# Optimization experiments

Measured on AMD Instinct MI355X. Metric: run time of the kernel, lower is better.

## Reference

```python
import jax, jax.numpy as jnp
import numpy as np

TEMP = 20.0     # args.temp
ATT_WT = 0.3    # args.att_wt
EPS = 1e-12     # torch F.normalize eps

L, B, C, H, W = 3, 2, 2048, 60, 60   # 3 layer4 bottleneck maps
CH = 256                              # merged feature channels for f_q/f_s


def setup_inputs() -> dict:
    key = jax.random.key(0)
    k1, k2, k3, k4, k5 = jax.random.split(key, 5)
    return {
        "fq_feats": jax.random.normal(k1, (L, B, C, H, W), dtype=jnp.float32),
        "fs_feats": jax.random.normal(k2, (L, B, C, H, W), dtype=jnp.float32),
        "f_q": jax.random.normal(k3, (B, CH, H, W), dtype=jnp.float32),
        "f_s": jax.random.normal(k4, (B, CH, H, W), dtype=jnp.float32),
        "corr_weight": jax.random.normal(k5, (L,), dtype=jnp.float32),
    }


def _l2_normalize(x, axis):
    # torch F.normalize(dim=1): x / max(||x||, eps)
    n = jnp.sqrt(jnp.sum(x * x, axis=axis, keepdims=True))
    return x / jnp.maximum(n, EPS)


def reference(fq_feats, fs_feats, f_q, f_s, corr_weight):
    b, ch, h, w = f_q.shape
    hw = h * w
    # per-scale channel-wise L2 normalize (cosine correlation)
    fqn = _l2_normalize(fq_feats, axis=2)   # [L,B,C,H,W]
    fsn = _l2_normalize(fs_feats, axis=2)
    # get_corr: pairwise cosine similarity volume per scale -> [B, L, hw_q, hw_s]
    fq_flat = fqn.reshape(fqn.shape[0], b, fqn.shape[2], hw)  # [L,B,C,hw]
    fs_flat = fsn.reshape(fsn.shape[0], b, fsn.shape[2], hw)
    corr = jnp.einsum('lbcq,lbcs->blqs', fq_flat, fs_flat)    # [B,L,hw,hw]
    # MatchNet corr_forward: 1x1 conv reducing match_ch -> 1, softmax over
    # support positions (scaled by temp), attend into v = f_s
    red = jnp.einsum('l,blqs->bqs', corr_weight, corr)        # [B,hw,hw]
    attn = jax.nn.softmax(red * TEMP, axis=-1)                # over support hw
    v = f_s.reshape(b, ch, hw)                                # [B,ch,hw]
    att_fq = jnp.einsum('bqs,bcs->bcq', attn, v).reshape(b, ch, h, w)
    fq = (f_q + att_fq * ATT_WT) / (1.0 + ATT_WT)
    return fq, att_fq
```

## Files before the change

### kernel.cpp

```cpp
#include <hip/hip_runtime.h>
#include <hip/hip_bf16.h>
#include <stdint.h>

#define L3D 3
#define BD 2
#define CD 2048
#define HW 3600
#define CH 256
#define HWP 3712
#define KD 6144
#define SP 3712
#define LB6 6
#define NPLANE 12
#define NT 48

typedef __attribute__((ext_vector_type(8))) short short8;
typedef __attribute__((ext_vector_type(4))) float f32x4;
typedef __attribute__((ext_vector_type(4))) int i32x4;
typedef __attribute__((ext_vector_type(8))) int i32x8;

__device__ __forceinline__ short f2bf(float v) {
  uint32_t x = __float_as_uint(v);
  uint32_t r = (x + 0x7FFFu + ((x >> 16) & 1u)) >> 16;
  return (short)(r & 0xFFFFu);
}

__device__ __forceinline__ float bf2f(short s) {
  return __uint_as_float(((uint32_t)(uint16_t)s) << 16);
}

__device__ __forceinline__ void load_lds16(const void* g, void* l) {
  __builtin_amdgcn_global_load_lds(
      (const __attribute__((address_space(1))) void*)g,
      (__attribute__((address_space(3))) void*)l, 16, 0, 0);
}

__global__ __launch_bounds__(256) void fnt_k(const float* __restrict__ fq,
                                             const float* __restrict__ fs,
                                             const float* __restrict__ cw,
                                             uint8_t* __restrict__ An,
                                             uint8_t* __restrict__ Bn) {
  const int j = blockIdx.y;
  const int qt = blockIdx.x * 64;
  const bool isq = (j < LB6);
  const int lb = isq ? j : j - LB6;
  const int l = lb / BD, b = lb % BD;
  const float* x = (isq ? fq : fs) + (size_t)lb * CD * HW;
  uint8_t* dst = isq ? An : Bn;

  const int tid = threadIdx.x;
  const int tx = tid & 63, part = tid >> 6;
  const int q = qt + tx;

  float s0 = 0.f, s1 = 0.f, s2 = 0.f, s3 = 0.f;
  if (q < HW) {
    const float* p = x + (size_t)part * 512 * HW + q;
    for (int c = 0; c < 512; c += 4) {
      float v0 = p[(size_t)(c + 0) * HW];
      float v1 = p[(size_t)(c + 1) * HW];
      float v2 = p[(size_t)(c + 2) * HW];
      float v3 = p[(size_t)(c + 3) * HW];
      s0 += v0 * v0; s1 += v1 * v1; s2 += v2 * v2; s3 += v3 * v3;
    }
  }
  __shared__ float buf[256];
  __shared__ float ivs[64];
  buf[tid] = (s0 + s1) + (s2 + s3);
  __syncthreads();
  if (tid < 64) {
    float t = buf[tid] + buf[tid + 64] + buf[tid + 128] + buf[tid + 192];
    const float scale = isq ? (cw[l] * 32.0f) : 32.0f;
    ivs[tid] = (1.f / fmaxf(sqrtf(t), 1e-12f)) * scale;
  }

  __shared__ float tile[64][65];
  const int wx = tid & 7, wy = tid >> 3;
  for (int ct = 0; ct < 32; ct++) {
    const float* px = x + (size_t)ct * 64 * HW;
    __syncthreads();
#pragma unroll
    for (int r = 0; r < 16; r++) {
      int cl = r * 4 + part;
      tile[cl][tx] = (q < HW) ? px[(size_t)cl * HW + q] : 0.f;
    }
    __syncthreads();
#pragma unroll
    for (int it = 0; it < 2; it++) {
      int qrow = wy + it * 32;
      int qq = qt + qrow;
      if (qq < HW) {
        float iv = ivs[qrow];
        float v[8];
#pragma unroll
        for (int jj = 0; jj < 8; jj++) v[jj] = tile[wx * 8 + jj][qrow] * iv;
        int lo = 0, hi = 0;
        lo = __builtin_amdgcn_cvt_pk_fp8_f32(v[0], v[1], lo, false);
        lo = __builtin_amdgcn_cvt_pk_fp8_f32(v[2], v[3], lo, true);
        hi = __builtin_amdgcn_cvt_pk_fp8_f32(v[4], v[5], hi, false);
        hi = __builtin_amdgcn_cvt_pk_fp8_f32(v[6], v[7], hi, true);
        int2 pk = make_int2(lo, hi);
        *reinterpret_cast<int2*>(dst + ((size_t)b * HWP + qq) * KD +
                                 (size_t)l * CD + ct * 64 + wx * 8) = pk;
      }
    }
  }
}

__global__ __launch_bounds__(512, 2) void gemm_main(const uint8_t* __restrict__ A,
                                                    const uint8_t* __restrict__ B,
                                                    __hip_bfloat16* __restrict__ C) {
  const int bz = blockIdx.y;
  const int lin = blockIdx.x;
  const int m_t = lin / 15, n_t = lin % 15;
  const int m0 = m_t * 256, n0 = n_t * 256;
  const int tid = threadIdx.x;
  const int lane = tid & 63;
  const int wv = tid >> 6;

  __shared__ uint8_t lA[2][256 * 128];
  __shared__ uint8_t lB[2][256 * 128];

  const uint8_t* gA = A + (size_t)bz * HWP * KD;
  const uint8_t* gB = B + (size_t)bz * HWP * KD;

  const int r_loc = tid >> 3;
  const int slot = tid & 7;
  const int csw = (slot - r_loc) & 7;
  const int wavebase = (tid & ~63) * 16;

  const int wr = (wv >> 2) * 128;
  const int wc = (wv & 3) * 64;
  const int ml = lane & 15;
  const int kg = lane >> 4;

  f32x4 acc[8][4];
#pragma unroll
  for (int i = 0; i < 8; i++)
#pragma unroll
    for (int jj = 0; jj < 4; jj++) acc[i][jj] = (f32x4){0.f, 0.f, 0.f, 0.f};

  auto stage = [&](int t, int bufi) {
    const int k0 = t * 128;
#pragma unroll
    for (int i = 0; i < 4; i++) {
      load_lds16(gA + (size_t)(m0 + i * 64 + r_loc) * KD + k0 + csw * 16,
                 &lA[bufi][i * 8192 + wavebase]);
      load_lds16(gB + (size_t)(n0 + i * 64 + r_loc) * KD + k0 + csw * 16,
                 &lB[bufi][i * 8192 + wavebase]);
    }
  };

  auto rdfrag = [&](const uint8_t* base, int row) -> i32x8 {
    const uint8_t* rp = base + (row << 7);
    i32x4 lo = *reinterpret_cast<const i32x4*>(rp + (((kg * 2)     + row) & 7) * 16);
    i32x4 hi = *reinterpret_cast<const i32x4*>(rp + (((kg * 2 + 1) + row) & 7) * 16);
    return __builtin_shufflevector(lo, hi, 0, 1, 2, 3, 4, 5, 6, 7);
  };

  stage(0, 0);
  asm volatile("s_waitcnt vmcnt(0)" ::: "memory");
  __builtin_amdgcn_s_barrier();

  for (int t = 0; t < NT; t++) {
    const int cur = t & 1;
    const uint8_t* pA = lA[cur];
    const uint8_t* pB = lB[cur];
    const bool st = (t + 1 < NT);
    i32x8 af[4], bfr[4];

#pragma unroll
    for (int x = 0; x < 4; x++) af[x] = rdfrag(pA, wr + x * 16 + ml);
#pragma unroll
    for (int x = 0; x < 2; x++) bfr[x] = rdfrag(pB, wc + x * 16 + ml);
    if (st) stage(t + 1, cur ^ 1);
    __builtin_amdgcn_s_barrier();
    asm volatile("s_waitcnt lgkmcnt(0)");
    __builtin_amdgcn_s_setprio(1);
#pragma unroll
    for (int mt = 0; mt < 4; mt++)
#pragma unroll
      for (int nt = 0; nt < 2; nt++)
        acc[mt][nt] = __builtin_amdgcn_mfma_scale_f32_16x16x128_f8f6f4(
            af[mt], bfr[nt], acc[mt][nt], 0, 0, 0, 0x7F7F7F7F, 0, 0x7F7F7F7F);
    __builtin_amdgcn_s_setprio(0);
    __builtin_amdgcn_s_barrier();

#pragma unroll
    for (int x = 2; x < 4; x++) bfr[x] = rdfrag(pB, wc + x * 16 + ml);
    __builtin_amdgcn_s_barrier();
    asm volatile("s_waitcnt lgkmcnt(0)");
    __builtin_amdgcn_s_setprio(1);
#pragma unroll
    for (int mt = 0; mt < 4; mt++)
#pragma unroll
      for (int nt = 2; nt < 4; nt++)
        acc[mt][nt] = __builtin_amdgcn_mfma_scale_f32_16x16x128_f8f6f4(
            af[mt], bfr[nt], acc[mt][nt], 0, 0, 0, 0x7F7F7F7F, 0, 0x7F7F7F7F);
    __builtin_amdgcn_s_setprio(0);
    __builtin_amdgcn_s_barrier();

#pragma unroll
    for (int x = 0; x < 4; x++) af[x] = rdfrag(pA, wr + 64 + x * 16 + ml);
    __builtin_amdgcn_s_barrier();
    asm volatile("s_waitcnt lgkmcnt(0)");
    __builtin_amdgcn_s_setprio(1);
#pragma unroll
    for (int mt = 0; mt < 4; mt++)
#pragma unroll
      for (int nt = 2; nt < 4; nt++)
        acc[4 + mt][nt] = __builtin_amdgcn_mfma_scale_f32_16x16x128_f8f6f4(
            af[mt], bfr[nt], acc[4 + mt][nt], 0, 0, 0, 0x7F7F7F7F, 0, 0x7F7F7F7F);
    __builtin_amdgcn_s_setprio(0);
    __builtin_amdgcn_s_barrier();

    __builtin_amdgcn_s_barrier();
    __builtin_amdgcn_s_setprio(1);
#pragma unroll
    for (int mt = 0; mt < 4; mt++)
#pragma unroll
      for (int nt = 0; nt < 2; nt++)
        acc[4 + mt][nt] = __builtin_amdgcn_mfma_scale_f32_16x16x128_f8f6f4(
            af[mt], bfr[nt], acc[4 + mt][nt], 0, 0, 0, 0x7F7F7F7F, 0, 0x7F7F7F7F);
    __builtin_amdgcn_s_setprio(0);
    if (st) asm volatile("s_waitcnt vmcnt(0)" ::: "memory");
    __builtin_amdgcn_s_barrier();
  }

  __hip_bfloat16* oc = C + (size_t)bz * HWP * SP;
  const int rq = (lane >> 4) * 4;
  const int cl = lane & 15;
#pragma unroll
  for (int mt = 0; mt < 8; mt++) {
    const int rb = m0 + wr + mt * 16 + rq;
#pragma unroll
    for (int nt = 0; nt < 4; nt++) {
      const int col = n0 + wc + nt * 16 + cl;
      if (col < SP) {
        f32x4 v = acc[mt][nt];
#pragma unroll
        for (int r = 0; r < 4; r++) {
          const int rr = rb + r;
          if (rr < HW) *reinterpret_cast<short*>(&oc[(size_t)rr * SP + col]) = f2bf(v[r]);
        }
      }
    }
  }
}

__global__ __launch_bounds__(256) void softmax_k(const __hip_bfloat16* __restrict__ red,
                                                 __hip_bfloat16* __restrict__ attn) {
  const int q = blockIdx.x;
  const int b = blockIdx.y;
  const __hip_bfloat16* row = red + ((size_t)b * HWP + q) * SP;
  __hip_bfloat16* orow = attn + ((size_t)b * HWP + q) * SP;
  const int tid = threadIdx.x;
  const int lane = tid & 63, wv = tid >> 6;
  const float SM = 20.0f / 1024.0f;

  float v0[8], v1[8];
  const int c1 = 256 + tid;
  const bool has1 = (c1 < 450);

  float mx = -3.4e38f;
  {
    short8 pk = *reinterpret_cast<const short8*>(&row[(size_t)tid * 8]);
#pragma unroll
    for (int j = 0; j < 8; j++) { v0[j] = bf2f(pk[j]); mx = fmaxf(mx, v0[j]); }
  }
  if (has1) {
    short8 pk = *reinterpret_cast<const short8*>(&row[(size_t)c1 * 8]);
#pragma unroll
    for (int j = 0; j < 8; j++) { v1[j] = bf2f(pk[j]); mx = fmaxf(mx, v1[j]); }
  }
  for (int off = 32; off > 0; off >>= 1) mx = fmaxf(mx, __shfl_down(mx, off, 64));
  __shared__ float sm[4];
  if (lane == 0) sm[wv] = mx;
  __syncthreads();
  mx = fmaxf(fmaxf(sm[0], sm[1]), fmaxf(sm[2], sm[3]));

  float sum = 0.f;
#pragma unroll
  for (int j = 0; j < 8; j++) { float e = __expf((v0[j] - mx) * SM); v0[j] = e; sum += e; }
  if (has1) {
#pragma unroll
    for (int j = 0; j < 8; j++) { float e = __expf((v1[j] - mx) * SM); v1[j] = e; sum += e; }
  }
  for (int off = 32; off > 0; off >>= 1) sum += __shfl_down(sum, off, 64);
  __syncthreads();
  if (lane == 0) sm[wv] = sum;
  __syncthreads();
  const float inv = 1.f / (sm[0] + sm[1] + sm[2] + sm[3]);

  {
    short8 o;
#pragma unroll
    for (int j = 0; j < 8; j++) o[j] = f2bf(v0[j] * inv);
    *reinterpret_cast<short8*>(&orow[(size_t)tid * 8]) = o;
  }
  if (has1) {
    short8 o;
#pragma unroll
    for (int j = 0; j < 8; j++) o[j] = f2bf(v1[j] * inv);
    *reinterpret_cast<short8*>(&orow[(size_t)c1 * 8]) = o;
  } else if (c1 < 464) {
    short8 z = {0, 0, 0, 0, 0, 0, 0, 0};
    *reinterpret_cast<short8*>(&orow[(size_t)c1 * 8]) = z;
  }
}

__global__ __launch_bounds__(256) void castv_k(const float* __restrict__ fs,
                                               __hip_bfloat16* __restrict__ vb) {
  const int idx = blockIdx.x * 256 + threadIdx.x;
  if (idx >= BD * CH * SP) return;
  const int s = idx % SP;
  const int bc = idx / SP;
  float v = (s < HW) ? fs[(size_t)bc * HW + s] : 0.f;
  *reinterpret_cast<short*>(&vb[idx]) = f2bf(v);
}

__global__ __launch_bounds__(256, 2) void pv_gemm(const __hip_bfloat16* __restrict__ A,
                                                  const __hip_bfloat16* __restrict__ B,
                                                  const float* __restrict__ fqin,
                                                  float* __restrict__ out) {
  const int bz = blockIdx.z;
  const int m0 = blockIdx.y * 128;
  const int n0 = blockIdx.x * 64;
  const int tid = threadIdx.x;
  const int lane = tid & 63;
  const int wv = tid >> 6;

  __shared__ __hip_bfloat16 lA[128 * 32];
  __shared__ __hip_bfloat16 lB[64 * 32];

  const __hip_bfloat16* gA = A + (size_t)bz * CH * SP;
  const __hip_bfloat16* gB = B + (size_t)bz * HWP * SP;

  const int r0 = tid >> 2;
  const int kc = (tid & 3) * 8;
  const int wb = (tid & ~63) * 8;

  const int wr = (wv >> 1) * 64;
  const int wc = (wv & 1) * 32;
  const int ml = lane & 15;
  const int kq = (lane >> 4) * 8;

  f32x4 acc[4][2];
#pragma unroll
  for (int i = 0; i < 4; i++)
#pragma unroll
    for (int jj = 0; jj < 2; jj++) acc[i][jj] = (f32x4){0.f, 0.f, 0.f, 0.f};

  for (int k0 = 0; k0 < SP; k0 += 32) {
    const __hip_bfloat16* pa0 = gA + (size_t)(m0 + r0) * SP + k0 + kc;
    const __hip_bfloat16* pb0 = gB + (size_t)(n0 + r0) * SP + k0 + kc;
    load_lds16(pa0, &lA[wb]);
    load_lds16(pa0 + (size_t)64 * SP, &lA[wb + 2048]);
    load_lds16(pb0, &lB[wb]);
    __syncthreads();

    short8 af[4], bfr[2];
#pragma unroll
    for (int t = 0; t < 4; t++)
      af[t] = *reinterpret_cast<const short8*>(&lA[(wr + t * 16 + ml) * 32 + kq]);
#pragma unroll
    for (int t = 0; t < 2; t++)
      bfr[t] = *reinterpret_cast<const short8*>(&lB[(wc + t * 16 + ml) * 32 + kq]);
#pragma unroll
    for (int mt = 0; mt < 4; mt++)
#pragma unroll
      for (int nt = 0; nt < 2; nt++)
        acc[mt][nt] = __builtin_amdgcn_mfma_f32_16x16x32_bf16(af[mt], bfr[nt], acc[mt][nt], 0, 0, 0);
    __syncthreads();
  }

  const size_t obase = (size_t)bz * CH * HW;
  const size_t attoff = (size_t)BD * CH * HW;
  const int rq = (lane >> 4) * 4;
  const int cl = lane & 15;
#pragma unroll
  for (int mt = 0; mt < 4; mt++) {
    const int rb = m0 + wr + mt * 16 + rq;
#pragma unroll
    for (int nt = 0; nt < 2; nt++) {
      const int col = n0 + wc + nt * 16 + cl;
      if (col < HW) {
        f32x4 v = acc[mt][nt];
#pragma unroll
        for (int r = 0; r < 4; r++) {
          const int c = rb + r;
          size_t oi = obase + (size_t)c * HW + col;
          float att = v[r];
          out[oi] = (fqin[oi] + 0.3f * att) * (1.0f / 1.3f);
          out[attoff + oi] = att;
        }
      }
    }
  }
}

extern "C" void kernel_launch(void* const* d_in, const int* in_sizes, int n_in,
                              void* d_out, int out_size, void* d_ws, size_t ws_size,
                              hipStream_t stream) {
  const float* fqf = (const float*)d_in[0];
  const float* fsf = (const float*)d_in[1];
  const float* f_q = (const float*)d_in[2];
  const float* f_s = (const float*)d_in[3];
  const float* cw  = (const float*)d_in[4];
  float* out = (float*)d_out;

  char* w = (char*)d_ws;
  uint8_t* An = (uint8_t*)w;   w += (size_t)BD * HWP * KD;
  uint8_t* Bn = (uint8_t*)w;   w += (size_t)BD * HWP * KD;
  __hip_bfloat16* red = (__hip_bfloat16*)w;
  __hip_bfloat16* attn = (__hip_bfloat16*)An;
  __hip_bfloat16* vb = (__hip_bfloat16*)(An + (size_t)BD * HWP * SP * 2);
  (void)ws_size; (void)in_sizes; (void)n_in; (void)out_size;

  fnt_k<<<dim3(57, NPLANE), 256, 0, stream>>>(fqf, fsf, cw, An, Bn);
  gemm_main<<<dim3(225, BD), 512, 0, stream>>>(An, Bn, red);
  softmax_k<<<dim3(HW, BD), 256, 0, stream>>>(red, attn);
  castv_k<<<(BD * CH * SP + 255) / 256, 256, 0, stream>>>(f_s, vb);
  pv_gemm<<<dim3(58, 2, BD), 256, 0, stream>>>(vb, attn, f_q, out);
}
```

Baseline: 869.7 us.

## Split normalize-transpose into separate norm and channel-parallel transpose kernels

The fused norm+transpose kernel ran only 57x12 blocks, each looping over all 2048 channels serially. The work is now split in two: a vectorized norm kernel computes partial sums of squares over 8 channel slices into a workspace, and a transpose/FP8-cast kernel gets a fourth grid dimension of 4 channel groups. This exposes more parallelism and gives the norm pass wider loads. The cost is an extra launch, a second full read of the inputs, and a small partial-sum buffer appended to the workspace.

```diff
diff --git a/kernel.cpp b/kernel.cpp
--- a/kernel.cpp
+++ b/kernel.cpp
@@ -10,6 +10,7 @@
 #define HWP 3712
 #define KD 6144
 #define SP 3712
+#define SP2 3840
 #define LB6 6
 #define NPLANE 12
 #define NT 48
@@ -35,13 +36,51 @@
       (__attribute__((address_space(3))) void*)l, 16, 0, 0);
 }
 
-__global__ __launch_bounds__(256) void fnt_k(const float* __restrict__ fq,
-                                             const float* __restrict__ fs,
-                                             const float* __restrict__ cw,
-                                             uint8_t* __restrict__ An,
-                                             uint8_t* __restrict__ Bn) {
+__global__ __launch_bounds__(256) void norm_k(const float* __restrict__ fq,
+                                              const float* __restrict__ fs,
+                                              float* __restrict__ part) {
+  const int qt = blockIdx.x * 256;
+  const int j = blockIdx.y;
+  const int cs = blockIdx.z;
+  const bool isq = (j < LB6);
+  const int lb = isq ? j : j - LB6;
+  const float* x = (isq ? fq : fs) + (size_t)lb * CD * HW;
+
+  const int tid = threadIdx.x;
+  const int qg = tid & 63;
+  const int cp = tid >> 6;
+  const int q4 = qt + qg * 4;
+
+  f32x4 a0 = (f32x4){0.f, 0.f, 0.f, 0.f};
+  f32x4 a1 = a0, a2 = a0, a3 = a0;
+  if (q4 < HW) {
+    const float* p = x + ((size_t)cs * 256 + cp) * HW + q4;
+    for (int i = 0; i < 64; i += 4) {
+      f32x4 v0 = *reinterpret_cast<const f32x4*>(p + (size_t)(i + 0) * 4 * HW);
+      f32x4 v1 = *reinterpret_cast<const f32x4*>(p + (size_t)(i + 1) * 4 * HW);
+      f32x4 v2 = *reinterpret_cast<const f32x4*>(p + (size_t)(i + 2) * 4 * HW);
+      f32x4 v3 = *reinterpret_cast<const f32x4*>(p + (size_t)(i + 3) * 4 * HW);
+      a0 += v0 * v0; a1 += v1 * v1; a2 += v2 * v2; a3 += v3 * v3;
+    }
+  }
+  f32x4 a = (a0 + a1) + (a2 + a3);
+
+  __shared__ float rb[4][256];
+  *reinterpret_cast<f32x4*>(&rb[cp][qg * 4]) = a;
+  __syncthreads();
+  float s = rb[0][tid] + rb[1][tid] + rb[2][tid] + rb[3][tid];
+  part[((size_t)cs * NPLANE + j) * SP2 + qt + tid] = s;
+}
+
+__global__ __launch_bounds__(256) void trans_k(const float* __restrict__ fq,
+                                               const float* __restrict__ fs,
+                                               const float* __restrict__ cw,
+                                               const float* __restrict__ part,
+                                               uint8_t* __restrict__ An,
+                                               uint8_t* __restrict__ Bn) {
   const int j = blockIdx.y;
   const int qt = blockIdx.x * 64;
+  const int cg = blockIdx.z;
   const bool isq = (j < LB6);
   const int lb = isq ? j : j - LB6;
   const int l = lb / BD, b = lb % BD;
@@ -49,38 +88,29 @@
   uint8_t* dst = isq ? An : Bn;
 
   const int tid = threadIdx.x;
-  const int tx = tid & 63, part = tid >> 6;
+
+  __shared__ float ivs[64];
+  if (tid < 64) {
+    const int q = qt + tid;
+    float s = 0.f;
+#pragma unroll
+    for (int cs = 0; cs < 8; cs++) s += part[((size_t)cs * NPLANE + j) * SP2 + q];
+    const float scale = isq ? (cw[l] * 32.0f) : 32.0f;
+    ivs[tid] = (1.f / fmaxf(sqrtf(s), 1e-12f)) * scale;
+  }
+
+  __shared__ float tile[64][65];
+  const int tx = tid & 63, partid = tid >> 6;
   const int q = qt + tx;
-
-  float s0 = 0.f, s1 = 0.f, s2 = 0.f, s3 = 0.f;
-  if (q < HW) {
-    const float* p = x + (size_t)part * 512 * HW + q;
-    for (int c = 0; c < 512; c += 4) {
-      float v0 = p[(size_t)(c + 0) * HW];
-      float v1 = p[(size_t)(c + 1) * HW];
-      float v2 = p[(size_t)(c + 2) * HW];
-      float v3 = p[(size_t)(c + 3) * HW];
-      s0 += v0 * v0; s1 += v1 * v1; s2 += v2 * v2; s3 += v3 * v3;
-    }
-  }
-  __shared__ float buf[256];
-  __shared__ float ivs[64];
-  buf[tid] = (s0 + s1) + (s2 + s3);
-  __syncthreads();
-  if (tid < 64) {
-    float t = buf[tid] + buf[tid + 64] + buf[tid + 128] + buf[tid + 192];
-    const float scale = isq ? (cw[l] * 32.0f) : 32.0f;
-    ivs[tid] = (1.f / fmaxf(sqrtf(t), 1e-12f)) * scale;
-  }
-
-  __shared__ float tile[64][65];
   const int wx = tid & 7, wy = tid >> 3;
-  for (int ct = 0; ct < 32; ct++) {
+
+  for (int t = 0; t < 8; t++) {
+    const int ct = cg * 8 + t;
     const float* px = x + (size_t)ct * 64 * HW;
     __syncthreads();
 #pragma unroll
     for (int r = 0; r < 16; r++) {
-      int cl = r * 4 + part;
+      int cl = r * 4 + partid;
       tile[cl][tx] = (q < HW) ? px[(size_t)cl * HW + q] : 0.f;
     }
     __syncthreads();
@@ -411,12 +441,14 @@
   char* w = (char*)d_ws;
   uint8_t* An = (uint8_t*)w;   w += (size_t)BD * HWP * KD;
   uint8_t* Bn = (uint8_t*)w;   w += (size_t)BD * HWP * KD;
-  __hip_bfloat16* red = (__hip_bfloat16*)w;
+  __hip_bfloat16* red = (__hip_bfloat16*)w;  w += (size_t)BD * HWP * SP * 2;
+  float* part = (float*)w;
   __hip_bfloat16* attn = (__hip_bfloat16*)An;
   __hip_bfloat16* vb = (__hip_bfloat16*)(An + (size_t)BD * HWP * SP * 2);
   (void)ws_size; (void)in_sizes; (void)n_in; (void)out_size;
 
-  fnt_k<<<dim3(57, NPLANE), 256, 0, stream>>>(fqf, fsf, cw, An, Bn);
+  norm_k<<<dim3(15, NPLANE, 8), 256, 0, stream>>>(fqf, fsf, part);
+  trans_k<<<dim3(57, NPLANE, 4), 256, 0, stream>>>(fqf, fsf, cw, part, An, Bn);
   gemm_main<<<dim3(225, BD), 512, 0, stream>>>(An, Bn, red);
   softmax_k<<<dim3(HW, BD), 256, 0, stream>>>(red, attn);
   castv_k<<<(BD * CH * SP + 255) / 256, 256, 0, stream>>>(f_s, vb);
```

After: 809.1 us. 1.07x faster.
